# Kernel optimization log

Measured on AMD Instinct MI355X. Metric: run time of the kernel, lower is better.

## Reference

```python
import jax, jax.numpy as jnp
import numpy as np

B, L, D, V, C = 16384, 50, 128, 91718, 11
H, HD, F = 4, 32, 6
NP = F * (F - 1) // 2  # 15 pairs
CIN = F * D + NP * D   # 2688


def setup_inputs() -> dict:
    key = jax.random.key(0)
    ks = jax.random.split(key, 32)
    inp = {}
    inp['item_id'] = jax.random.randint(ks[0], (B,), 0, V)
    inp['item_mm'] = jax.random.normal(ks[1], (B, D), dtype=jnp.float32)
    inp['likes'] = jax.random.randint(ks[2], (B,), 0, C)
    inp['views'] = jax.random.randint(ks[3], (B,), 0, C)
    inp['item_seq'] = jax.random.randint(ks[4], (B, L), 0, V)
    g = lambda k, shape, s: (jax.random.normal(k, shape, dtype=jnp.float32) * s)
    inp['item_emb'] = g(ks[5], (V, D), 0.02).at[0].set(0.0)  # padding_idx=0
    inp['cate_emb'] = g(ks[6], (C, D), 0.02)
    inp['mm_w'] = g(ks[7], (D, D), (2.0 / D) ** 0.5)
    inp['mm_b'] = jnp.zeros((D,), jnp.float32)
    inp['ln_g'] = jnp.ones((D,), jnp.float32)
    inp['ln_b'] = jnp.zeros((D,), jnp.float32)
    inp['gnn_W'] = g(ks[8], (H, D, HD), (2.0 / (D + HD)) ** 0.5 * 1.414)
    inp['gnn_a'] = g(ks[9], (H, 2 * HD, 1), 0.1)
    inp['se_w1'] = g(ks[10], (F, F // 2), 0.4)
    inp['se_b1'] = jnp.zeros((F // 2,), jnp.float32)
    inp['se_w2'] = g(ks[11], (F // 2, F), 0.4)
    inp['se_b2'] = jnp.zeros((F,), jnp.float32)
    inp['bi_W'] = g(ks[12], (F - 1, D, D), (2.0 / (2 * D)) ** 0.5)
    inp['mlp_w1'] = g(ks[13], (CIN, 512), (2.0 / CIN) ** 0.5)
    inp['mlp_b1'] = jnp.zeros((512,), jnp.float32)
    inp['bn1_g'] = jnp.ones((512,), jnp.float32)
    inp['bn1_b'] = jnp.zeros((512,), jnp.float32)
    inp['mlp_w2'] = g(ks[14], (512, 256), (2.0 / 512) ** 0.5)
    inp['mlp_b2'] = jnp.zeros((256,), jnp.float32)
    inp['bn2_g'] = jnp.ones((256,), jnp.float32)
    inp['bn2_b'] = jnp.zeros((256,), jnp.float32)
    inp['mlp_w3'] = g(ks[15], (256, 1), (2.0 / 256) ** 0.5)
    inp['mlp_b3'] = jnp.zeros((1,), jnp.float32)
    return inp


def _forward(item_id, item_mm, likes, views, item_seq,
             item_emb, cate_emb, mm_w, mm_b, ln_g, ln_b,
             gnn_W, gnn_a, se_w1, se_b1, se_w2, se_b2, bi_W,
             mlp_w1, mlp_b1, bn1_g, bn1_b, mlp_w2, mlp_b2, bn2_g, bn2_b,
             mlp_w3, mlp_b3):
    bsz = item_id.shape[0]
    eps = 1e-5

    user_feat = jnp.zeros((bsz, D), item_mm.dtype)
    like_feat = cate_emb[likes]
    view_feat = cate_emb[views]
    id_feat = item_emb[item_id]

    # mm_proj: Linear -> LayerNorm -> GELU (exact)
    y = item_mm @ mm_w + mm_b
    mu = y.mean(-1, keepdims=True)
    var = y.var(-1, keepdims=True)
    y = (y - mu) * jax.lax.rsqrt(var + eps) * ln_g + ln_b
    img_feat = jax.nn.gelu(y, approximate=False)

    # masked mean pooling of history
    seq_emb = item_emb[item_seq]                          # [B,L,D]
    mask = item_seq == 0
    seq_emb = jnp.where(mask[..., None], 0.0, seq_emb)
    cnt = jnp.clip(jnp.sum((~mask).astype(seq_emb.dtype), axis=1, keepdims=True), 1.0)
    hist_feat = seq_emb.sum(1) / cnt

    x = jnp.stack([user_feat, like_feat, view_feat, id_feat, img_feat, hist_feat], axis=1)  # [B,6,D]

    # GAT over 6-node fully-connected feature graph
    hp = jnp.einsum('bni,hio->bnho', x, gnn_W)            # [B,6,H,HD]
    a1 = gnn_a[:, :HD, 0]                                  # [H,HD]
    a2 = gnn_a[:, HD:, 0]
    ei = jnp.einsum('bnhd,hd->bhn', hp, a1)
    ej = jnp.einsum('bnhd,hd->bhn', hp, a2)
    e = ei[:, :, :, None] + ej[:, :, None, :]             # [B,H,6,6]
    e = jnp.where(e > 0, e, 0.2 * e)                       # LeakyReLU(0.2)
    att = jax.nn.softmax(e, axis=-1)                       # dropout off (eval)
    h_new = jnp.einsum('bhnm,bmho->bnho', att, hp).reshape(bsz, F, D)
    gnn_feat = jax.nn.elu(h_new + x)                       # in_dim == out_dim

    # SENet
    z = gnn_feat.mean(-1)                                  # [B,6]
    w = jax.nn.sigmoid(jax.nn.relu(z @ se_w1 + se_b1) @ se_w2 + se_b2)
    s = gnn_feat * w[..., None]

    # Bilinear ('each'): vid_i = s_i @ W_i, pairs (i,j), j>i
    vid = jnp.einsum('bfd,fde->bfe', s[:, :F - 1], bi_W)   # [B,5,D]
    p = jnp.stack([vid[:, i] * s[:, j] for i in range(F - 1) for j in range(i + 1, F)], axis=1)  # [B,15,D]

    c = jnp.concatenate([gnn_feat.reshape(bsz, -1), p.reshape(bsz, -1)], axis=1)  # [B,2688]

    # MLP with eval-mode BatchNorm (running mean 0, var 1) and dropout off
    bn = lambda t, g_, b_: t * (g_ / jnp.sqrt(1.0 + eps)) + b_
    h1 = jax.nn.gelu(bn(c @ mlp_w1 + mlp_b1, bn1_g, bn1_b), approximate=False)
    h2 = jax.nn.gelu(bn(h1 @ mlp_w2 + mlp_b2, bn2_g, bn2_b), approximate=False)
    out = jax.nn.sigmoid(h2 @ mlp_w3 + mlp_b3)
    return out.squeeze(-1)


def reference(item_id, item_mm, likes, views, item_seq,
              item_emb, cate_emb, mm_w, mm_b, ln_g, ln_b,
              gnn_W, gnn_a, se_w1, se_b1, se_w2, se_b2, bi_W,
              mlp_w1, mlp_b1, bn1_g, bn1_b, mlp_w2, mlp_b2, bn2_g, bn2_b,
              mlp_w3, mlp_b3):
    return _forward(item_id, item_mm, likes, views, item_seq,
                    item_emb, cate_emb, mm_w, mm_b, ln_g, ln_b,
                    gnn_W, gnn_a, se_w1, se_b1, se_w2, se_b2, bi_W,
                    mlp_w1, mlp_b1, bn1_g, bn1_b, mlp_w2, mlp_b2, bn2_g, bn2_b,
                    mlp_w3, mlp_b3)
```

## Files before the change

### kernel.cpp

```cpp
#include <hip/hip_runtime.h>
#include <hip/hip_bf16.h>
#include <cstdint>
#include <cstddef>

#define BB 16384

typedef float  floatx4 __attribute__((ext_vector_type(4)));
typedef __bf16 bf16x8  __attribute__((ext_vector_type(8)));

__device__ __forceinline__ unsigned short f2bf(float f) {
  union { float f; unsigned int u; } v; v.f = f;
  unsigned int r = v.u + 0x7FFFu + ((v.u >> 16) & 1u);
  return (unsigned short)(r >> 16);
}
__device__ __forceinline__ float bf2f(unsigned short h) {
  union { unsigned int u; float f; } v; v.u = ((unsigned int)h) << 16;
  return v.f;
}
__device__ __forceinline__ float gelu_exact(float x) {
  return 0.5f * x * (1.0f + erff(x * 0.7071067811865475f));
}

#define ALOAD16(g, l) \
  __builtin_amdgcn_global_load_lds((const __attribute__((address_space(1))) void*)(g), \
                                   (__attribute__((address_space(3))) void*)(l), 16, 0, 0)

__global__ void k_pack(const float* __restrict__ mm_w, const float* __restrict__ gnn_W,
                       const float* __restrict__ bi_W, const float* __restrict__ item_mm,
                       unsigned short* __restrict__ mmwt, unsigned short* __restrict__ wallt,
                       unsigned short* __restrict__ biwt, unsigned short* __restrict__ immb)
{
  const int total = 2211840;
  for (int id = blockIdx.x * 256 + threadIdx.x; id < total; id += gridDim.x * 256) {
    if (id < 16384) {
      int n = id / 128, k = id % 128;
      mmwt[id] = f2bf(mm_w[k * 128 + n]);
    } else if (id < 32768) {
      int l = id - 16384; int nc = l / 128, k = l % 128;
      wallt[l] = f2bf(gnn_W[(nc >> 5) * 4096 + k * 32 + (nc & 31)]);
    } else if (id < 114688) {
      int l = id - 32768; int f = l / 16384, rr = l % 16384, e = rr / 128, d = rr % 128;
      biwt[l] = f2bf(bi_W[f * 16384 + d * 128 + e]);
    } else {
      int l = id - 114688;
      immb[l] = f2bf(item_mm[l]);
    }
  }
}

__global__ __launch_bounds__(256)
void k_cvt(const float* __restrict__ in, unsigned short* __restrict__ out, int n4)
{
  int i = blockIdx.x * 256 + threadIdx.x;
  if (i < n4) {
    float4 v = ((const float4*)in)[i];
    ushort4 o; o.x = f2bf(v.x); o.y = f2bf(v.y); o.z = f2bf(v.z); o.w = f2bf(v.w);
    ((ushort4*)out)[i] = o;
  }
}

__global__ __launch_bounds__(256)
void k_transp(const float* __restrict__ in, unsigned short* __restrict__ out, int R, int C)
{
  __shared__ float tile[64][65];
  const int c0 = blockIdx.x * 64, r0 = blockIdx.y * 64;
  const int lr = threadIdx.x >> 6;
  const int lc = threadIdx.x & 63;
  #pragma unroll
  for (int i = 0; i < 16; i++) {
    int r = lr + i * 4;
    tile[r][lc] = in[(size_t)(r0 + r) * C + c0 + lc];
  }
  __syncthreads();
  #pragma unroll
  for (int i = 0; i < 16; i++) {
    int c = lr + i * 4;
    out[(size_t)(c0 + c) * R + r0 + lc] = f2bf(tile[lc][c]);
  }
}

template<int EPI, bool SWZ>
__global__ __launch_bounds__(256)
void gemm_bt(const unsigned short* __restrict__ A, int lda,
             const unsigned short* __restrict__ Bt, int ldb,
             void* __restrict__ Cp, int ldc, int K,
             const float* __restrict__ bias, const float* __restrict__ bng,
             const float* __restrict__ bnb)
{
  int bx = blockIdx.x, by = blockIdx.y;
  if constexpr (SWZ) {
    int p = by * gridDim.x + bx;
    int xcd = p & 7, slot = p >> 3;
    bx = slot % gridDim.x;
    by = xcd * (gridDim.y >> 3) + slot / gridDim.x;
  }
  const int n0 = bx * 128;
  const int m0 = by * 128;
  __shared__ __align__(16) unsigned short As[128 * 64];
  __shared__ __align__(16) unsigned short Bs[128 * 64];
  const int t = threadIdx.x;
  const int lane = t & 63, w = t >> 6;
  const int wm = w & 1, wn = w >> 1;
  const int lr = lane & 15, lq = lane >> 4;

  floatx4 acc[4][4];
  #pragma unroll
  for (int a = 0; a < 4; a++)
    #pragma unroll
    for (int b = 0; b < 4; b++) acc[a][b] = (floatx4){0.f, 0.f, 0.f, 0.f};

  const int srow = lane >> 3;
  const int schk = (lane & 7) ^ srow;
  const unsigned short* Ag = A + (size_t)(m0 + w * 32 + srow) * lda + schk * 8;
  const unsigned short* Bg = Bt + (size_t)(n0 + w * 32 + srow) * ldb + schk * 8;
  unsigned short* AsW = As + w * 32 * 64;
  unsigned short* BsW = Bs + w * 32 * 64;

  for (int k0 = 0; k0 < K; k0 += 64) {
    __syncthreads();
    #pragma unroll
    for (int q = 0; q < 4; q++) {
      ALOAD16(Ag + k0 + (size_t)(q * 8) * lda, AsW + q * 512);
      ALOAD16(Bg + k0 + (size_t)(q * 8) * ldb, BsW + q * 512);
    }
    __syncthreads();
    #pragma unroll
    for (int ko = 0; ko < 2; ko++) {
      bf16x8 af[4], bfv[4];
      #pragma unroll
      for (int mt = 0; mt < 4; mt++) {
        const int row = wm * 64 + mt * 16 + lr;
        const int pc = (ko * 4 + lq) ^ (lr & 7);
        af[mt] = __builtin_bit_cast(bf16x8, *(const uint4*)&As[row * 64 + pc * 8]);
      }
      #pragma unroll
      for (int nt = 0; nt < 4; nt++) {
        const int row = wn * 64 + nt * 16 + lr;
        const int pc = (ko * 4 + lq) ^ (lr & 7);
        bfv[nt] = __builtin_bit_cast(bf16x8, *(const uint4*)&Bs[row * 64 + pc * 8]);
      }
      #pragma unroll
      for (int mt = 0; mt < 4; mt++)
        #pragma unroll
        for (int nt = 0; nt < 4; nt++)
          acc[mt][nt] = __builtin_amdgcn_mfma_f32_16x16x32_bf16(af[mt], bfv[nt], acc[mt][nt], 0, 0, 0);
    }
  }

  #pragma unroll
  for (int mt = 0; mt < 4; mt++)
    #pragma unroll
    for (int nt = 0; nt < 4; nt++)
      #pragma unroll
      for (int i = 0; i < 4; i++) {
        const int cm = m0 + wm * 64 + mt * 16 + lq * 4 + i;
        const int cn = n0 + wn * 64 + nt * 16 + lr;
        float v = acc[mt][nt][i];
        size_t idx = (size_t)cm * ldc + cn;
        if constexpr (EPI == 0) {
          ((float*)Cp)[idx] = v + bias[cn];
        } else if constexpr (EPI == 2) {
          ((unsigned short*)Cp)[idx] = f2bf(v);
        } else {
          float tt = v + bias[cn];
          tt = tt * (bng[cn] * 0.9999950000374997f) + bnb[cn];
          ((unsigned short*)Cp)[idx] = f2bf(gelu_exact(tt));
        }
      }
}

__global__ __launch_bounds__(256)
void gemm_vid(const unsigned short* __restrict__ sbb, const unsigned short* __restrict__ biwt,
              unsigned short* __restrict__ c)
{
  const int z = blockIdx.z;
  const int m0 = blockIdx.y * 128;
  __shared__ __align__(16) unsigned short smem[128 * 130];
  unsigned short* As = smem;
  unsigned short* Bs = smem + 8192;
  const int t = threadIdx.x;
  const int lane = t & 63, w = t >> 6;
  const int wm = w & 1, wn = w >> 1;
  const int lr = lane & 15, lq = lane >> 4;

  floatx4 acc[4][4];
  #pragma unroll
  for (int a = 0; a < 4; a++)
    #pragma unroll
    for (int b = 0; b < 4; b++) acc[a][b] = (floatx4){0.f, 0.f, 0.f, 0.f};

  const int srow = lane >> 3;
  const int schk = (lane & 7) ^ srow;
  const unsigned short* Ag = sbb + (size_t)(m0 + w * 32 + srow) * 768 + z * 128 + schk * 8;
  const unsigned short* Bg = biwt + z * 16384 + (size_t)(w * 32 + srow) * 128 + schk * 8;
  unsigned short* AsW = As + w * 32 * 64;
  unsigned short* BsW = Bs + w * 32 * 64;

  for (int k0 = 0; k0 < 128; k0 += 64) {
    __syncthreads();
    #pragma unroll
    for (int q = 0; q < 4; q++) {
      ALOAD16(Ag + k0 + (size_t)(q * 8) * 768, AsW + q * 512);
      ALOAD16(Bg + k0 + (size_t)(q * 8) * 128, BsW + q * 512);
    }
    __syncthreads();
    #pragma unroll
    for (int ko = 0; ko < 2; ko++) {
      bf16x8 af[4], bfv[4];
      #pragma unroll
      for (int mt = 0; mt < 4; mt++) {
        const int row = wm * 64 + mt * 16 + lr;
        const int pc = (ko * 4 + lq) ^ (lr & 7);
        af[mt] = __builtin_bit_cast(bf16x8, *(const uint4*)&As[row * 64 + pc * 8]);
      }
      #pragma unroll
      for (int nt = 0; nt < 4; nt++) {
        const int row = wn * 64 + nt * 16 + lr;
        const int pc = (ko * 4 + lq) ^ (lr & 7);
        bfv[nt] = __builtin_bit_cast(bf16x8, *(const uint4*)&Bs[row * 64 + pc * 8]);
      }
      #pragma unroll
      for (int mt = 0; mt < 4; mt++)
        #pragma unroll
        for (int nt = 0; nt < 4; nt++)
          acc[mt][nt] = __builtin_amdgcn_mfma_f32_16x16x32_bf16(af[mt], bfv[nt], acc[mt][nt], 0, 0, 0);
    }
  }

  __syncthreads();
  #pragma unroll
  for (int mt = 0; mt < 4; mt++)
    #pragma unroll
    for (int nt = 0; nt < 4; nt++)
      #pragma unroll
      for (int i = 0; i < 4; i++) {
        const int rr = wm * 64 + mt * 16 + lq * 4 + i;
        const int cc = wn * 64 + nt * 16 + lr;
        smem[rr * 130 + cc] = f2bf(acc[mt][nt][i]);
      }
  __syncthreads();

  const int pb0[5] = {0, 5, 9, 12, 14};
  const int npairs = 5 - z;
  const int tot = 128 * 32 * npairs;
  for (int e = t; e < tot; e += 256) {
    const int g  = e & 31;
    const int rp = e >> 5;
    const int p  = rp % npairs;
    const int r  = rp / npairs;
    ushort4 vv = *(const ushort4*)&smem[r * 130 + g * 4];
    ushort4 sv = *(const ushort4*)&sbb[(size_t)(m0 + r) * 768 + (z + 1 + p) * 128 + g * 4];
    ushort4 o;
    o.x = f2bf(bf2f(vv.x) * bf2f(sv.x));
    o.y = f2bf(bf2f(vv.y) * bf2f(sv.y));
    o.z = f2bf(bf2f(vv.z) * bf2f(sv.z));
    o.w = f2bf(bf2f(vv.w) * bf2f(sv.w));
    *(ushort4*)&c[(size_t)(m0 + r) * 2688 + 768 + (size_t)(pb0[z] + p) * 128 + g * 4] = o;
  }
}

__global__ __launch_bounds__(256)
void k_feat(const int* __restrict__ item_id, const int* __restrict__ likes,
            const int* __restrict__ views, const int* __restrict__ item_seq,
            const unsigned short* __restrict__ iembb, const float* __restrict__ cate_emb,
            unsigned short* __restrict__ xb)
{
  const int b = blockIdx.x * 4 + (threadIdx.x >> 6);
  const int lane = threadIdx.x & 63;
  const int half = lane >> 5, ql = lane & 31;
  const size_t base = (size_t)b * 768;
  const int li = likes[b], vi = views[b], id = item_id[b];

  int idxs[25];
  #pragma unroll
  for (int j = 0; j < 25; j++) idxs[j] = item_seq[b * 50 + half + 2 * j];

  float4 hs = make_float4(0.f, 0.f, 0.f, 0.f);
  float cnt = 0.f;
  #pragma unroll
  for (int j = 0; j < 25; j++) {
    const int idx = idxs[j];
    if (idx != 0) {
      cnt += 1.0f;
      ushort4 v = *(const ushort4*)&iembb[(size_t)idx * 128 + ql * 4];
      hs.x += bf2f(v.x); hs.y += bf2f(v.y); hs.z += bf2f(v.z); hs.w += bf2f(v.w);
    }
  }
  cnt  += __shfl_xor(cnt, 32, 64);
  hs.x += __shfl_xor(hs.x, 32, 64);
  hs.y += __shfl_xor(hs.y, 32, 64);
  hs.z += __shfl_xor(hs.z, 32, 64);
  hs.w += __shfl_xor(hs.w, 32, 64);
  const float ic = 1.0f / fmaxf(cnt, 1.0f);

  *(unsigned int*)&xb[base + lane * 2] = 0u;

  {
    const float4 v = *(const float4*)&cate_emb[(size_t)(half ? vi : li) * 128 + ql * 4];
    ushort4 o; o.x = f2bf(v.x); o.y = f2bf(v.y); o.z = f2bf(v.z); o.w = f2bf(v.w);
    *(ushort4*)&xb[base + 128 + half * 128 + ql * 4] = o;
  }
  if (half == 0) {
    *(ushort4*)&xb[base + 384 + ql * 4] =
        *(const ushort4*)&iembb[(size_t)id * 128 + ql * 4];
  } else {
    ushort4 o; o.x = f2bf(hs.x * ic); o.y = f2bf(hs.y * ic);
               o.z = f2bf(hs.z * ic); o.w = f2bf(hs.w * ic);
    *(ushort4*)&xb[base + 640 + ql * 4] = o;
  }
}

__global__ __launch_bounds__(256)
void k_ln(const float* __restrict__ y, const float* __restrict__ ln_g,
          const float* __restrict__ ln_b, unsigned short* __restrict__ xb)
{
  const int b = blockIdx.x * 4 + (threadIdx.x >> 6);
  const int lane = threadIdx.x & 63;
  float v0 = y[(size_t)b * 128 + lane], v1 = y[(size_t)b * 128 + lane + 64];
  float s = v0 + v1, s2 = v0 * v0 + v1 * v1;
  #pragma unroll
  for (int o = 32; o > 0; o >>= 1) { s += __shfl_xor(s, o, 64); s2 += __shfl_xor(s2, o, 64); }
  float mu  = s * (1.0f / 128.0f);
  float var = s2 * (1.0f / 128.0f) - mu * mu;
  float rs  = rsqrtf(var + 1e-5f);
  float t0 = (v0 - mu) * rs * ln_g[lane]      + ln_b[lane];
  float t1 = (v1 - mu) * rs * ln_g[lane + 64] + ln_b[lane + 64];
  xb[(size_t)b * 768 + 512 + lane]      = f2bf(gelu_exact(t0));
  xb[(size_t)b * 768 + 512 + lane + 64] = f2bf(gelu_exact(t1));
}

__global__ __launch_bounds__(256)
void k_att(const unsigned short* __restrict__ hp, const unsigned short* __restrict__ xb,
           const float* __restrict__ gnn_a, const float* __restrict__ se_w1,
           const float* __restrict__ se_b1, const float* __restrict__ se_w2,
           const float* __restrict__ se_b2, unsigned short* __restrict__ c,
           unsigned short* __restrict__ sb)
{
  __shared__ float hps[4][6][128];
  __shared__ float eis[4][4][6], ejs[4][4][6];
  __shared__ float atts[4][4][6][6];
  const int wv = threadIdx.x >> 6, lane = threadIdx.x & 63;
  const int b = blockIdx.x * 4 + wv;

  #pragma unroll
  for (int n = 0; n < 6; n++) {
    unsigned int pk = *(const unsigned int*)&hp[((size_t)b * 6 + n) * 128 + lane * 2];
    float2 f; f.x = bf2f((unsigned short)(pk & 0xFFFFu));
              f.y = bf2f((unsigned short)(pk >> 16));
    *(float2*)&hps[wv][n][lane * 2] = f;
  }
  __syncthreads();

  if (lane < 24) {
    int h = lane & 3, n = lane >> 2;
    float e1 = 0.f, e2 = 0.f;
    for (int o = 0; o < 32; o++) {
      float v = hps[wv][n][h * 32 + o];
      e1 += v * gnn_a[h * 64 + o];
      e2 += v * gnn_a[h * 64 + 32 + o];
    }
    eis[wv][h][n] = e1; ejs[wv][h][n] = e2;
  }
  __syncthreads();

  if (lane < 24) {
    int h = lane & 3, i = lane >> 2;
    float ev[6]; float mx = -1e30f;
    #pragma unroll
    for (int j = 0; j < 6; j++) {
      float e = eis[wv][h][i] + ejs[wv][h][j];
      e = e > 0.f ? e : 0.2f * e;
      ev[j] = e; mx = fmaxf(mx, e);
    }
    float ssum = 0.f;
    #pragma unroll
    for (int j = 0; j < 6; j++) { ev[j] = expf(ev[j] - mx); ssum += ev[j]; }
    float inv = 1.0f / ssum;
    #pragma unroll
    for (int j = 0; j < 6; j++) atts[wv][h][i][j] = ev[j] * inv;
  }
  __syncthreads();

  const int h = lane >> 4;
  float g0[6], g1[6], zz[6];
  #pragma unroll
  for (int n = 0; n < 6; n++) {
    float hn0 = 0.f, hn1 = 0.f;
    #pragma unroll
    for (int m = 0; m < 6; m++) {
      float a = atts[wv][h][n][m];
      float2 v = *(const float2*)&hps[wv][m][lane * 2];
      hn0 += a * v.x; hn1 += a * v.y;
    }
    unsigned int xp = *(const unsigned int*)&xb[(size_t)b * 768 + n * 128 + lane * 2];
    float a0 = hn0 + bf2f((unsigned short)(xp & 0xFFFFu));
    float a1 = hn1 + bf2f((unsigned short)(xp >> 16));
    a0 = a0 > 0.f ? a0 : expm1f(a0);
    a1 = a1 > 0.f ? a1 : expm1f(a1);
    g0[n] = a0; g1[n] = a1;
    float zacc = a0 + a1;
    #pragma unroll
    for (int o = 32; o > 0; o >>= 1) zacc += __shfl_xor(zacc, o, 64);
    zz[n] = zacc * (1.0f / 128.0f);
  }

  float rr[3];
  #pragma unroll
  for (int j = 0; j < 3; j++) {
    float a = se_b1[j];
    #pragma unroll
    for (int n = 0; n < 6; n++) a += zz[n] * se_w1[n * 3 + j];
    rr[j] = fmaxf(a, 0.f);
  }
  float wse[6];
  #pragma unroll
  for (int n = 0; n < 6; n++) {
    float a = se_b2[n];
    #pragma unroll
    for (int j = 0; j < 3; j++) a += rr[j] * se_w2[j * 6 + n];
    wse[n] = 1.0f / (1.0f + expf(-a));
  }

  #pragma unroll
  for (int n = 0; n < 6; n++) {
    unsigned int pc = (unsigned int)f2bf(g0[n]) | ((unsigned int)f2bf(g1[n]) << 16);
    unsigned int ps = (unsigned int)f2bf(g0[n] * wse[n]) | ((unsigned int)f2bf(g1[n] * wse[n]) << 16);
    *(unsigned int*)&c[(size_t)b * 2688 + n * 128 + lane * 2]  = pc;
    *(unsigned int*)&sb[(size_t)b * 768 + n * 128 + lane * 2]  = ps;
  }
}

__global__ __launch_bounds__(256)
void k_out(const unsigned short* __restrict__ h2, const float* __restrict__ w3,
           const float* __restrict__ b3, float* __restrict__ out)
{
  const int b = blockIdx.x * 4 + (threadIdx.x >> 6);
  const int lane = threadIdx.x & 63;
  ushort4 v = *(const ushort4*)&h2[(size_t)b * 256 + lane * 4];
  float a = bf2f(v.x) * w3[lane * 4]     + bf2f(v.y) * w3[lane * 4 + 1]
          + bf2f(v.z) * w3[lane * 4 + 2] + bf2f(v.w) * w3[lane * 4 + 3];
  #pragma unroll
  for (int o = 32; o > 0; o >>= 1) a += __shfl_xor(a, o, 64);
  if (lane == 0) out[b] = 1.0f / (1.0f + expf(-(a + b3[0])));
}

#define OFF_MMWT   0ull
#define OFF_WALLT  32768ull
#define OFF_BIWT   65536ull
#define OFF_W1T    229376ull
#define OFF_W2T    2981888ull
#define OFF_IMMB   3244032ull
#define OFF_XB     7438336ull
#define OFF_HP     32604160ull
#define OFF_SB     57769984ull
#define OFF_C      82935808ull
#define OFF_H2     171016192ull
#define OFF_IEMB   179404800ull

extern "C" void kernel_launch(void* const* d_in, const int* in_sizes, int n_in,
                              void* d_out, int out_size, void* d_ws, size_t ws_size,
                              hipStream_t stream)
{
  const int*   item_id  = (const int*)  d_in[0];
  const float* item_mm  = (const float*)d_in[1];
  const int*   likes    = (const int*)  d_in[2];
  const int*   views    = (const int*)  d_in[3];
  const int*   item_seq = (const int*)  d_in[4];
  const float* item_emb = (const float*)d_in[5];
  const float* cate_emb = (const float*)d_in[6];
  const float* mm_w     = (const float*)d_in[7];
  const float* mm_b     = (const float*)d_in[8];
  const float* ln_g     = (const float*)d_in[9];
  const float* ln_b     = (const float*)d_in[10];
  const float* gnn_W    = (const float*)d_in[11];
  const float* gnn_a    = (const float*)d_in[12];
  const float* se_w1    = (const float*)d_in[13];
  const float* se_b1    = (const float*)d_in[14];
  const float* se_w2    = (const float*)d_in[15];
  const float* se_b2    = (const float*)d_in[16];
  const float* bi_W     = (const float*)d_in[17];
  const float* mlp_w1   = (const float*)d_in[18];
  const float* mlp_b1   = (const float*)d_in[19];
  const float* bn1_g    = (const float*)d_in[20];
  const float* bn1_b    = (const float*)d_in[21];
  const float* mlp_w2   = (const float*)d_in[22];
  const float* mlp_b2   = (const float*)d_in[23];
  const float* bn2_g    = (const float*)d_in[24];
  const float* bn2_b    = (const float*)d_in[25];
  const float* mlp_w3   = (const float*)d_in[26];
  const float* mlp_b3   = (const float*)d_in[27];
  float* out = (float*)d_out;

  char* ws = (char*)d_ws;
  unsigned short* mmwt  = (unsigned short*)(ws + OFF_MMWT);
  unsigned short* wallt = (unsigned short*)(ws + OFF_WALLT);
  unsigned short* biwt  = (unsigned short*)(ws + OFF_BIWT);
  unsigned short* w1t   = (unsigned short*)(ws + OFF_W1T);
  unsigned short* w2t   = (unsigned short*)(ws + OFF_W2T);
  unsigned short* immb  = (unsigned short*)(ws + OFF_IMMB);
  unsigned short* xb    = (unsigned short*)(ws + OFF_XB);
  unsigned short* hpb   = (unsigned short*)(ws + OFF_HP);
  unsigned short* sbb   = (unsigned short*)(ws + OFF_SB);
  float*          yb    = (float*)         (ws + OFF_SB);
  unsigned short* cbuf  = (unsigned short*)(ws + OFF_C);
  unsigned short* h1b   = (unsigned short*)(ws + OFF_XB);
  unsigned short* h2b   = (unsigned short*)(ws + OFF_H2);
  unsigned short* iembb = (unsigned short*)(ws + OFF_IEMB);

  k_pack<<<2048, 256, 0, stream>>>(mm_w, gnn_W, bi_W, item_mm, mmwt, wallt, biwt, immb);
  k_cvt<<<(2934976 + 255) / 256, 256, 0, stream>>>(item_emb, iembb, 2934976);
  k_transp<<<dim3(8, 42), 256, 0, stream>>>(mlp_w1, w1t, 2688, 512);
  k_transp<<<dim3(4, 8),  256, 0, stream>>>(mlp_w2, w2t, 512, 256);
  k_feat<<<BB / 4, 256, 0, stream>>>(item_id, likes, views, item_seq, iembb, cate_emb, xb);
  gemm_bt<0, false><<<dim3(1, 128, 1), 256, 0, stream>>>(immb, 128, mmwt, 128,
      yb, 128, 128, mm_b, nullptr, nullptr);
  k_ln<<<BB / 4, 256, 0, stream>>>(yb, ln_g, ln_b, xb);
  gemm_bt<2, false><<<dim3(1, 768, 1), 256, 0, stream>>>(xb, 128, wallt, 128,
      hpb, 128, 128, nullptr, nullptr, nullptr);
  k_att<<<BB / 4, 256, 0, stream>>>(hpb, xb, gnn_a, se_w1, se_b1, se_w2, se_b2, cbuf, sbb);
  gemm_vid<<<dim3(1, 128, 5), 256, 0, stream>>>(sbb, biwt, cbuf);
  gemm_bt<3, true><<<dim3(4, 128, 1), 256, 0, stream>>>(cbuf, 2688, w1t, 2688,
      h1b, 512, 2688, mlp_b1, bn1_g, bn1_b);
  gemm_bt<3, true><<<dim3(2, 128, 1), 256, 0, stream>>>(h1b, 512, w2t, 512,
      h2b, 256, 512, mlp_b2, bn2_g, bn2_b);
  k_out<<<BB / 4, 256, 0, stream>>>(h2b, mlp_w3, mlp_b3, out);
}
```

Baseline: 367.3 us.

## Use 512-thread GEMM blocks with templated BM and merge embedding conversion into pack

The GEMM kernel is templated on the M tile size and moves to 8 waves per 512-thread block. The wave layout and the split of LDS loads between A and B rows are derived from BM, and the smaller-N GEMMs switch to BM=64 with twice as many blocks. Separately, the item_emb bf16 conversion is folded into k_pack, removing one kernel launch. Each block now has more waves, but each wave holds fewer accumulator tiles, which trades per-wave MFMA reuse for parallelism.

```diff
diff --git a/kernel.cpp b/kernel.cpp
--- a/kernel.cpp
+++ b/kernel.cpp
@@ -27,10 +27,12 @@
 
 __global__ void k_pack(const float* __restrict__ mm_w, const float* __restrict__ gnn_W,
                        const float* __restrict__ bi_W, const float* __restrict__ item_mm,
+                       const float* __restrict__ item_emb,
                        unsigned short* __restrict__ mmwt, unsigned short* __restrict__ wallt,
-                       unsigned short* __restrict__ biwt, unsigned short* __restrict__ immb)
-{
-  const int total = 2211840;
+                       unsigned short* __restrict__ biwt, unsigned short* __restrict__ immb,
+                       unsigned short* __restrict__ iembb)
+{
+  const int total = 2211840 + 2934976;
   for (int id = blockIdx.x * 256 + threadIdx.x; id < total; id += gridDim.x * 256) {
     if (id < 16384) {
       int n = id / 128, k = id % 128;
@@ -41,21 +43,15 @@
     } else if (id < 114688) {
       int l = id - 32768; int f = l / 16384, rr = l % 16384, e = rr / 128, d = rr % 128;
       biwt[l] = f2bf(bi_W[f * 16384 + d * 128 + e]);
-    } else {
+    } else if (id < 2211840) {
       int l = id - 114688;
       immb[l] = f2bf(item_mm[l]);
-    }
-  }
-}
-
-__global__ __launch_bounds__(256)
-void k_cvt(const float* __restrict__ in, unsigned short* __restrict__ out, int n4)
-{
-  int i = blockIdx.x * 256 + threadIdx.x;
-  if (i < n4) {
-    float4 v = ((const float4*)in)[i];
-    ushort4 o; o.x = f2bf(v.x); o.y = f2bf(v.y); o.z = f2bf(v.z); o.w = f2bf(v.w);
-    ((ushort4*)out)[i] = o;
+    } else {
+      int l = id - 2211840;
+      float4 v = ((const float4*)item_emb)[l];
+      ushort4 o; o.x = f2bf(v.x); o.y = f2bf(v.y); o.z = f2bf(v.z); o.w = f2bf(v.w);
+      ((ushort4*)iembb)[l] = o;
+    }
   }
 }
 
@@ -79,14 +75,21 @@
   }
 }
 
-template<int EPI, bool SWZ>
-__global__ __launch_bounds__(256)
+template<int BM, int EPI, bool SWZ>
+__global__ __launch_bounds__(512)
 void gemm_bt(const unsigned short* __restrict__ A, int lda,
              const unsigned short* __restrict__ Bt, int ldb,
              void* __restrict__ Cp, int ldc, int K,
              const float* __restrict__ bias, const float* __restrict__ bng,
              const float* __restrict__ bnb)
 {
+  constexpr int WGM = BM / 64;
+  constexpr int WGN = 8 / WGM;
+  constexpr int TN  = 128 / WGN;
+  constexpr int NT  = TN / 16;
+  constexpr int NRW = (BM + 128) / 8;
+  constexpr int ISS = NRW / 8;
+
   int bx = blockIdx.x, by = blockIdx.y;
   if constexpr (SWZ) {
     int p = by * gridDim.x + bx;
@@ -95,38 +98,40 @@
     by = xcd * (gridDim.y >> 3) + slot / gridDim.x;
   }
   const int n0 = bx * 128;
-  const int m0 = by * 128;
-  __shared__ __align__(16) unsigned short As[128 * 64];
+  const int m0 = by * BM;
+  __shared__ __align__(16) unsigned short As[BM * 64];
   __shared__ __align__(16) unsigned short Bs[128 * 64];
   const int t = threadIdx.x;
   const int lane = t & 63, w = t >> 6;
-  const int wm = w & 1, wn = w >> 1;
+  const int wm = w % WGM, wn = w / WGM;
   const int lr = lane & 15, lq = lane >> 4;
 
-  floatx4 acc[4][4];
+  floatx4 acc[4][NT];
   #pragma unroll
   for (int a = 0; a < 4; a++)
     #pragma unroll
-    for (int b = 0; b < 4; b++) acc[a][b] = (floatx4){0.f, 0.f, 0.f, 0.f};
+    for (int b = 0; b < NT; b++) acc[a][b] = (floatx4){0.f, 0.f, 0.f, 0.f};
 
   const int srow = lane >> 3;
   const int schk = (lane & 7) ^ srow;
-  const unsigned short* Ag = A + (size_t)(m0 + w * 32 + srow) * lda + schk * 8;
-  const unsigned short* Bg = Bt + (size_t)(n0 + w * 32 + srow) * ldb + schk * 8;
-  unsigned short* AsW = As + w * 32 * 64;
-  unsigned short* BsW = Bs + w * 32 * 64;
+  const int rb0 = w * NRW;
 
   for (int k0 = 0; k0 < K; k0 += 64) {
     __syncthreads();
     #pragma unroll
-    for (int q = 0; q < 4; q++) {
-      ALOAD16(Ag + k0 + (size_t)(q * 8) * lda, AsW + q * 512);
-      ALOAD16(Bg + k0 + (size_t)(q * 8) * ldb, BsW + q * 512);
+    for (int q = 0; q < ISS; q++) {
+      const int rb = rb0 + q * 8;
+      if (rb < BM) {
+        ALOAD16(A + (size_t)(m0 + rb + srow) * lda + k0 + schk * 8, As + rb * 64);
+      } else {
+        const int rbb = rb - BM;
+        ALOAD16(Bt + (size_t)(n0 + rbb + srow) * ldb + k0 + schk * 8, Bs + rbb * 64);
+      }
     }
     __syncthreads();
     #pragma unroll
     for (int ko = 0; ko < 2; ko++) {
-      bf16x8 af[4], bfv[4];
+      bf16x8 af[4], bfv[NT];
       #pragma unroll
       for (int mt = 0; mt < 4; mt++) {
         const int row = wm * 64 + mt * 16 + lr;
@@ -134,15 +139,15 @@
         af[mt] = __builtin_bit_cast(bf16x8, *(const uint4*)&As[row * 64 + pc * 8]);
       }
       #pragma unroll
-      for (int nt = 0; nt < 4; nt++) {
-        const int row = wn * 64 + nt * 16 + lr;
+      for (int nt = 0; nt < NT; nt++) {
+        const int row = wn * TN + nt * 16 + lr;
         const int pc = (ko * 4 + lq) ^ (lr & 7);
         bfv[nt] = __builtin_bit_cast(bf16x8, *(const uint4*)&Bs[row * 64 + pc * 8]);
       }
       #pragma unroll
       for (int mt = 0; mt < 4; mt++)
         #pragma unroll
-        for (int nt = 0; nt < 4; nt++)
+        for (int nt = 0; nt < NT; nt++)
           acc[mt][nt] = __builtin_amdgcn_mfma_f32_16x16x32_bf16(af[mt], bfv[nt], acc[mt][nt], 0, 0, 0);
     }
   }
@@ -150,11 +155,11 @@
   #pragma unroll
   for (int mt = 0; mt < 4; mt++)
     #pragma unroll
-    for (int nt = 0; nt < 4; nt++)
+    for (int nt = 0; nt < NT; nt++)
       #pragma unroll
       for (int i = 0; i < 4; i++) {
         const int cm = m0 + wm * 64 + mt * 16 + lq * 4 + i;
-        const int cn = n0 + wn * 64 + nt * 16 + lr;
+        const int cn = n0 + wn * TN + nt * 16 + lr;
         float v = acc[mt][nt][i];
         size_t idx = (size_t)cm * ldc + cn;
         if constexpr (EPI == 0) {
@@ -507,21 +512,21 @@
   unsigned short* h2b   = (unsigned short*)(ws + OFF_H2);
   unsigned short* iembb = (unsigned short*)(ws + OFF_IEMB);
 
-  k_pack<<<2048, 256, 0, stream>>>(mm_w, gnn_W, bi_W, item_mm, mmwt, wallt, biwt, immb);
-  k_cvt<<<(2934976 + 255) / 256, 256, 0, stream>>>(item_emb, iembb, 2934976);
+  k_pack<<<4096, 256, 0, stream>>>(mm_w, gnn_W, bi_W, item_mm, item_emb,
+                                   mmwt, wallt, biwt, immb, iembb);
   k_transp<<<dim3(8, 42), 256, 0, stream>>>(mlp_w1, w1t, 2688, 512);
   k_transp<<<dim3(4, 8),  256, 0, stream>>>(mlp_w2, w2t, 512, 256);
   k_feat<<<BB / 4, 256, 0, stream>>>(item_id, likes, views, item_seq, iembb, cate_emb, xb);
-  gemm_bt<0, false><<<dim3(1, 128, 1), 256, 0, stream>>>(immb, 128, mmwt, 128,
+  gemm_bt<64, 0, false><<<dim3(1, 256), 512, 0, stream>>>(immb, 128, mmwt, 128,
       yb, 128, 128, mm_b, nullptr, nullptr);
   k_ln<<<BB / 4, 256, 0, stream>>>(yb, ln_g, ln_b, xb);
-  gemm_bt<2, false><<<dim3(1, 768, 1), 256, 0, stream>>>(xb, 128, wallt, 128,
+  gemm_bt<128, 2, false><<<dim3(1, 768), 512, 0, stream>>>(xb, 128, wallt, 128,
       hpb, 128, 128, nullptr, nullptr, nullptr);
   k_att<<<BB / 4, 256, 0, stream>>>(hpb, xb, gnn_a, se_w1, se_b1, se_w2, se_b2, cbuf, sbb);
   gemm_vid<<<dim3(1, 128, 5), 256, 0, stream>>>(sbb, biwt, cbuf);
-  gemm_bt<3, true><<<dim3(4, 128, 1), 256, 0, stream>>>(cbuf, 2688, w1t, 2688,
+  gemm_bt<128, 3, true><<<dim3(4, 128), 512, 0, stream>>>(cbuf, 2688, w1t, 2688,
       h1b, 512, 2688, mlp_b1, bn1_g, bn1_b);
-  gemm_bt<3, true><<<dim3(2, 128, 1), 256, 0, stream>>>(h1b, 512, w2t, 512,
+  gemm_bt<64, 3, true><<<dim3(2, 256), 512, 0, stream>>>(h1b, 512, w2t, 512,
       h2b, 256, 512, mlp_b2, bn2_g, bn2_b);
   k_out<<<BB / 4, 256, 0, stream>>>(h2b, mlp_w3, mlp_b3, out);
 }
```

New measurement: 349.6 us. 1.05x faster.
